# Performance work log

Hardware: AMD Instinct MI355X
Metric: run time of the kernel (lower is better)

The kernel has to match this reference:

```python
import jax, jax.numpy as jnp
import numpy as np

N_NODES = 50000
N_RAND_EDGES = 800000
NEG_SLOPE = 0.2


def gat_conv(h, src, dst, W, attn_l, attn_r, bias, res_W=None, act=False):
    # DGL GATConv semantics: fc -> per-node attn halves -> per-edge leaky_relu
    # logits -> segment softmax over destination -> weighted scatter-sum.
    N = h.shape[0]
    H, D = attn_l.shape
    feat = (h @ W).reshape(N, H, D)                      # (N,H,D)
    el = (feat * attn_l[None]).sum(-1)                   # (N,H)
    er = (feat * attn_r[None]).sum(-1)                   # (N,H)
    e = jax.nn.leaky_relu(el[src] + er[dst], NEG_SLOPE)  # (E,H)
    emax = jax.ops.segment_max(e, dst, num_segments=N)   # (N,H)
    ee = jnp.exp(e - emax[dst])                          # (E,H)
    denom = jax.ops.segment_sum(ee, dst, num_segments=N)
    alpha = ee / denom[dst]                              # (E,H)
    msg = feat[src] * alpha[:, :, None]                  # (E,H,D) dominant traffic
    rst = jax.ops.segment_sum(msg, dst, num_segments=N)  # (N,H,D)
    if res_W is not None:
        rst = rst + (h @ res_W).reshape(N, H, D)
    rst = rst + bias.reshape(1, H, D)
    if act:
        rst = jax.nn.relu(rst)
    return rst


def setup_inputs() -> dict:
    key = jax.random.key(0)
    ks = jax.random.split(key, 20)
    x = jax.random.normal(ks[0], (N_NODES, 64), dtype=jnp.float32)
    src_r = jax.random.randint(ks[1], (N_RAND_EDGES,), 0, N_NODES, dtype=jnp.int32)
    dst_r = jax.random.randint(ks[2], (N_RAND_EDGES,), 0, N_NODES, dtype=jnp.int32)
    loops = jnp.arange(N_NODES, dtype=jnp.int32)
    src = jnp.concatenate([src_r, loops])   # self-loops: no zero in-degree
    dst = jnp.concatenate([dst_r, loops])
    s = 0.1
    p = lambda k, shp: jax.random.normal(k, shp, dtype=jnp.float32) * s
    return {
        "x": x, "src": src, "dst": dst,
        # layer 1: in=64 -> hid=32, heads=4, relu, no residual
        "W1": p(ks[3], (64, 128)), "al1": p(ks[4], (4, 32)), "ar1": p(ks[5], (4, 32)),
        "b1": jnp.zeros((128,), jnp.float32),
        # layer 2: in=128 -> hid=32, heads=4, relu, residual
        "W2": p(ks[6], (128, 128)), "al2": p(ks[7], (4, 32)), "ar2": p(ks[8], (4, 32)),
        "b2": jnp.zeros((128,), jnp.float32), "resW2": p(ks[9], (128, 128)),
        # layer 3: in=128 -> out=1, heads=6, no activation, residual
        "W3": p(ks[10], (128, 6)), "al3": p(ks[11], (6, 1)), "ar3": p(ks[12], (6, 1)),
        "b3": jnp.zeros((6,), jnp.float32), "resW3": p(ks[13], (128, 6)),
    }


def reference(x, src, dst, W1, al1, ar1, b1, W2, al2, ar2, b2, resW2,
              W3, al3, ar3, b3, resW3):
    h = gat_conv(x, src, dst, W1, al1, ar1, b1, None, act=True)
    h = h.reshape(h.shape[0], -1)                        # flatten heads
    h = gat_conv(h, src, dst, W2, al2, ar2, b2, resW2, act=True)
    h = h.reshape(h.shape[0], -1)
    h = gat_conv(h, src, dst, W3, al3, ar3, b3, resW3, act=False)
    return h.mean(axis=1)                                # mean over heads -> (N, out)
```

## Files before the change

### kernel.cpp

```cpp
#include <hip/hip_runtime.h>
#include <hip/hip_fp16.h>

#define NEG 0.2f
#define BUCKET_SHIFT 7
#define CAP 3200
#define PCHUNK 4096

typedef _Float16 h8 __attribute__((ext_vector_type(8)));
typedef float f4v __attribute__((ext_vector_type(4)));

template <int K>
__global__ __launch_bounds__(256) void gemm_el_k(const float* __restrict__ A,
                                                 const float* __restrict__ W,
                                                 const float* __restrict__ al,
                                                 const float* __restrict__ ar,
                                                 __half* __restrict__ feat_h,
                                                 float* __restrict__ el,
                                                 float* __restrict__ er, int N) {
    __shared__ float As[64 * K];
    const int c = threadIdx.x & 31;
    const int rg = threadIdx.x >> 5;
    const int row0 = blockIdx.x << 6;
    const int K4 = K >> 2;

    const float4* Av = (const float4*)A;
    float4* AsV = (float4*)As;
    for (int idx = threadIdx.x; idx < 16 * K; idx += 256) {
        int rr = idx / K4, kk4 = idx - rr * K4;
        int row = row0 + rr;
        float4 v = make_float4(0.f, 0.f, 0.f, 0.f);
        if (row < N) v = Av[(size_t)row * K4 + kk4];
        AsV[rr * K4 + kk4] = v;
    }
    __syncthreads();

    const float4* Wv = (const float4*)W;
    float4 acc[8];
#pragma unroll
    for (int i = 0; i < 8; i++) acc[i] = make_float4(0.f, 0.f, 0.f, 0.f);

    for (int k4 = 0; k4 < K4; k4++) {
        float4 a[8];
#pragma unroll
        for (int i = 0; i < 8; i++) a[i] = AsV[(rg * 8 + i) * K4 + k4];
#pragma unroll
        for (int kk = 0; kk < 4; kk++) {
            float4 w = Wv[((k4 << 2) + kk) * 32 + c];
#pragma unroll
            for (int i = 0; i < 8; i++) {
                float av = kk == 0 ? a[i].x : kk == 1 ? a[i].y : kk == 2 ? a[i].z : a[i].w;
                acc[i].x += av * w.x;
                acc[i].y += av * w.y;
                acc[i].z += av * w.z;
                acc[i].w += av * w.w;
            }
        }
    }

    __half2* Fh2 = (__half2*)feat_h;
#pragma unroll
    for (int i = 0; i < 8; i++) {
        int row = row0 + rg * 8 + i;
        if (row < N) {
            size_t o = ((size_t)row << 6) + (c << 1);
            Fh2[o] = __floats2half2_rn(acc[i].x, acc[i].y);
            Fh2[o + 1] = __floats2half2_rn(acc[i].z, acc[i].w);
        }
    }

    float4 alv = ((const float4*)al)[c];
    float4 arv = ((const float4*)ar)[c];
    float pel[8], per_[8];
#pragma unroll
    for (int i = 0; i < 8; i++) {
        pel[i] = acc[i].x * alv.x + acc[i].y * alv.y + acc[i].z * alv.z + acc[i].w * alv.w;
        per_[i] = acc[i].x * arv.x + acc[i].y * arv.y + acc[i].z * arv.z + acc[i].w * arv.w;
    }
#pragma unroll
    for (int m = 1; m < 8; m <<= 1) {
#pragma unroll
        for (int i = 0; i < 8; i++) {
            pel[i] += __shfl_xor(pel[i], m);
            per_[i] += __shfl_xor(per_[i], m);
        }
    }
    if ((c & 7) == 0) {
        int h = c >> 3;
#pragma unroll
        for (int i = 0; i < 8; i++) {
            int row = row0 + rg * 8 + i;
            if (row < N) {
                el[(row << 2) + h] = pel[i];
                er[(row << 2) + h] = per_[i];
            }
        }
    }
}

__global__ __launch_bounds__(256) void wconv_k(const float* __restrict__ W2,
                                               const float* __restrict__ rW2,
                                               float4* __restrict__ W2f,
                                               float4* __restrict__ rW2f) {
    int c = blockIdx.x * 256 + threadIdx.x;
    int which = c >> 11;
    int cc = c & 2047;
    int kb = cc >> 9, rem = cc & 511, t = rem >> 6, lane = rem & 63;
    int n = (t << 4) + (lane & 15);
    int k0 = (kb << 5) + ((lane >> 4) << 3);
    const float* S = which ? rW2 : W2;
    h8 v;
#pragma unroll
    for (int i = 0; i < 8; i++) v[i] = (_Float16)S[(k0 + i) * 128 + n];
    ((h8*)(which ? rW2f : W2f))[cc] = v;
}

#define MFMA_STAGE_AND_LOOP()                                                   \
    const int tid = threadIdx.x;                                                \
    const int row0 = blockIdx.x << 6;                                           \
    for (int i = tid; i < 2048; i += 256) WsF[i] = Wf[i];                       \
    const float4* Afv = (const float4*)A;                                       \
    for (int idx = tid; idx < 1024; idx += 256) {                               \
        int r = idx >> 4, kc = idx & 15;                                        \
        float4 v = make_float4(0.f, 0.f, 0.f, 0.f);                             \
        int row = row0 + r;                                                     \
        if (row < N) v = Afv[(size_t)row * 16 + kc];                            \
        int d = ((r >> 4) * 4 + (kc >> 2)) * 64 + (kc & 3) * 16 + (r & 15);     \
        AsF[d] = v;                                                             \
    }                                                                           \
    __syncthreads();                                                            \
    const int w = tid >> 6;                                                     \
    const int lane = tid & 63;                                                  \
    const h8* Ah = (const h8*)AsF;                                              \
    const h8* Wh = (const h8*)WsF;                                              \
    f4v acc[8];                                                                 \
    _Pragma("unroll") for (int t = 0; t < 8; t++) acc[t] = (f4v){0.f, 0.f, 0.f, 0.f}; \
    _Pragma("unroll") for (int kb = 0; kb < 4; kb++) {                          \
        h8 af = Ah[(w * 4 + kb) * 64 + lane];                                   \
        _Pragma("unroll") for (int t = 0; t < 8; t++) {                         \
            h8 bf = Wh[(kb * 8 + t) * 64 + lane];                               \
            acc[t] = __builtin_amdgcn_mfma_f32_16x16x32_f16(af, bf, acc[t], 0, 0, 0); \
        }                                                                       \
    }                                                                           \
    const int c16 = lane & 15;                                                  \
    const int rg = lane >> 4;

__global__ __launch_bounds__(256) void mfma_el_k(const _Float16* __restrict__ A,
                                                 const float4* __restrict__ Wf,
                                                 const float* __restrict__ al,
                                                 const float* __restrict__ ar,
                                                 _Float16* __restrict__ feat,
                                                 float* __restrict__ el,
                                                 float* __restrict__ er, int N) {
    __shared__ float4 WsF[2048];
    __shared__ float4 AsF[1024];
    MFMA_STAGE_AND_LOOP()

    float alv[8], arv[8];
#pragma unroll
    for (int t = 0; t < 8; t++) {
        alv[t] = al[(t << 4) + c16];
        arv[t] = ar[(t << 4) + c16];
    }
    float pel[4][4], per_[4][4];
#pragma unroll
    for (int j = 0; j < 4; j++)
#pragma unroll
        for (int hh = 0; hh < 4; hh++) {
            pel[j][hh] = acc[2 * hh][j] * alv[2 * hh] + acc[2 * hh + 1][j] * alv[2 * hh + 1];
            per_[j][hh] = acc[2 * hh][j] * arv[2 * hh] + acc[2 * hh + 1][j] * arv[2 * hh + 1];
        }
#pragma unroll
    for (int m = 1; m < 16; m <<= 1)
#pragma unroll
        for (int j = 0; j < 4; j++)
#pragma unroll
            for (int hh = 0; hh < 4; hh++) {
                pel[j][hh] += __shfl_xor(pel[j][hh], m);
                per_[j][hh] += __shfl_xor(per_[j][hh], m);
            }
    if (c16 == 0) {
#pragma unroll
        for (int j = 0; j < 4; j++) {
            int row = row0 + (w << 4) + (rg << 2) + j;
            if (row < N) {
                ((float4*)el)[row] = make_float4(pel[j][0], pel[j][1], pel[j][2], pel[j][3]);
                ((float4*)er)[row] = make_float4(per_[j][0], per_[j][1], per_[j][2], per_[j][3]);
            }
        }
    }

    _Float16* As2 = (_Float16*)AsF + (w << 11);
#pragma unroll
    for (int t = 0; t < 8; t++)
#pragma unroll
        for (int j = 0; j < 4; j++)
            As2[((rg << 2) + j) * 128 + (t << 4) + c16] = (_Float16)acc[t][j];
    __asm__ volatile("s_waitcnt lgkmcnt(0)" ::: "memory");
    const float4* As2v = (const float4*)As2;
    float4* featv = (float4*)feat;
#pragma unroll
    for (int ii = 0; ii < 4; ii++) {
        int ch = ii * 64 + lane;
        int row = row0 + (w << 4) + (ch >> 4);
        if (row < N) featv[(size_t)row * 16 + (ch & 15)] = As2v[ch];
    }
}

__global__ __launch_bounds__(256) void mfma_res_k(const _Float16* __restrict__ A,
                                                  const float4* __restrict__ Wf,
                                                  const _Float16* __restrict__ rsth,
                                                  const float* __restrict__ b2,
                                                  const float* __restrict__ W3,
                                                  const float* __restrict__ resW3,
                                                  const float* __restrict__ b3,
                                                  float* __restrict__ feat3,
                                                  float* __restrict__ res3, int N) {
    __shared__ float4 WsF[2048];
    __shared__ float4 AsF[1024];
    MFMA_STAGE_AND_LOOP()

    float4* As2v = (float4*)AsF + (w << 8);
#pragma unroll
    for (int ii = 0; ii < 4; ii++) {
        int ch = ii * 64 + lane;
        int row = row0 + (w << 4) + (ch >> 4);
        float4 v = make_float4(0.f, 0.f, 0.f, 0.f);
        if (row < N) v = ((const float4*)rsth)[(size_t)row * 16 + (ch & 15)];
        As2v[ch] = v;
    }
    __asm__ volatile("s_waitcnt lgkmcnt(0)" ::: "memory");
    const _Float16* As2 = (const _Float16*)As2v;

    float b2v[8];
#pragma unroll
    for (int t = 0; t < 8; t++) b2v[t] = b2[(t << 4) + c16];

    float hv[8][4];
#pragma unroll
    for (int t = 0; t < 8; t++)
#pragma unroll
        for (int j = 0; j < 4; j++) {
            float rv = (float)As2[((rg << 2) + j) * 128 + (t << 4) + c16];
            hv[t][j] = fmaxf(acc[t][j] + rv + b2v[t], 0.f);
        }

    float f3[4][6], r3[4][6];
#pragma unroll
    for (int j = 0; j < 4; j++)
#pragma unroll
        for (int h = 0; h < 6; h++) {
            f3[j][h] = 0.f;
            r3[j][h] = 0.f;
        }
#pragma unroll
    for (int t = 0; t < 8; t++) {
        int col = (t << 4) + c16;
        const float* w3p = W3 + col * 6;
        const float* rwp = resW3 + col * 6;
#pragma unroll
        for (int h = 0; h < 6; h++) {
            float w3 = w3p[h], rw = rwp[h];
#pragma unroll
            for (int j = 0; j < 4; j++) {
                f3[j][h] = fmaf(hv[t][j], w3, f3[j][h]);
                r3[j][h] = fmaf(hv[t][j], rw, r3[j][h]);
            }
        }
    }
#pragma unroll
    for (int m = 1; m < 16; m <<= 1)
#pragma unroll
        for (int j = 0; j < 4; j++)
#pragma unroll
            for (int h = 0; h < 6; h++) {
                f3[j][h] += __shfl_xor(f3[j][h], m);
                r3[j][h] += __shfl_xor(r3[j][h], m);
            }
    if (c16 == 0) {
#pragma unroll
        for (int j = 0; j < 4; j++) {
            int row = row0 + (w << 4) + (rg << 2) + j;
            if (row < N) {
#pragma unroll
                for (int h = 0; h < 6; h++) {
                    feat3[row * 6 + h] = f3[j][h];
                    res3[row * 6 + h] = r3[j][h] + b3[h];
                }
            }
        }
    }
}

__global__ __launch_bounds__(256) void partition_k(const int* __restrict__ src,
                                                   const int* __restrict__ dst,
                                                   int* __restrict__ cursor,
                                                   unsigned* __restrict__ part,
                                                   int E, int NB) {
    __shared__ unsigned stash[PCHUNK];
    __shared__ int hist[512];
    __shared__ int base[512];
    const int tid = threadIdx.x;
    const int e0 = blockIdx.x * PCHUNK;

    for (int i = tid; i < NB; i += 256) hist[i] = 0;
    __syncthreads();

    for (int i = tid; i < PCHUNK; i += 256) {
        int e = e0 + i;
        unsigned pk = 0xFFFFFFFFu;
        if (e < E) {
            int d = dst[e];
            pk = ((unsigned)d << 16) | (unsigned)src[e];
            atomicAdd(&hist[d >> BUCKET_SHIFT], 1);
        }
        stash[i] = pk;
    }
    __syncthreads();

    for (int i = tid; i < NB; i += 256) {
        int hcnt = hist[i];
        base[i] = hcnt ? atomicAdd(&cursor[i], hcnt) : 0;
        hist[i] = 0;
    }
    __syncthreads();

    for (int i = tid; i < PCHUNK; i += 256) {
        unsigned pk = stash[i];
        if (pk != 0xFFFFFFFFu) {
            int b = pk >> (16 + BUCKET_SHIFT);
            int r = base[b] + atomicAdd(&hist[b], 1);
            if (r < CAP) part[(size_t)b * CAP + r] = pk;
        }
    }
}

__global__ __launch_bounds__(256) void bucket_csr_k(const int* __restrict__ cursor,
                                                    const unsigned* __restrict__ part,
                                                    int* __restrict__ csr_src,
                                                    int* __restrict__ row_beg,
                                                    int* __restrict__ row_end,
                                                    int N) {
    __shared__ int cnt[128], sc[128], ex[128], cur[128];
    __shared__ int lcsr[CAP];
    const int b = blockIdx.x;
    const int tid = threadIdx.x;
    int m = cursor[b];
    m = m < CAP ? m : CAP;
    if (tid < 128) cnt[tid] = 0;
    __syncthreads();

    const unsigned* pp = part + (size_t)b * CAP;
    for (int i = tid; i < m; i += 256) atomicAdd(&cnt[(pp[i] >> 16) & 127], 1);
    __syncthreads();

    if (tid < 128) sc[tid] = cnt[tid];
    __syncthreads();
    for (int off = 1; off < 128; off <<= 1) {
        int t = (tid < 128 && tid >= off) ? sc[tid - off] : 0;
        __syncthreads();
        if (tid < 128) sc[tid] += t;
        __syncthreads();
    }
    if (tid < 128) {
        ex[tid] = sc[tid] - cnt[tid];
        cur[tid] = 0;
    }
    __syncthreads();

    for (int i = tid; i < m; i += 256) {
        unsigned pk = pp[i];
        int dlo = (pk >> 16) & 127;
        int r = atomicAdd(&cur[dlo], 1);
        lcsr[ex[dlo] + r] = (int)(pk & 0xFFFFu);
    }
    __syncthreads();

    const int gbase = b * CAP;
    for (int i = tid; i < m; i += 256) csr_src[gbase + i] = lcsr[i];
    int n = (b << BUCKET_SHIFT) + tid;
    if (tid < 128 && n < N) {
        row_beg[n] = gbase + ex[tid];
        row_end[n] = gbase + sc[tid];
    }
}

template <bool BR>
__global__ __launch_bounds__(256) void pull2_k(const int* __restrict__ row_beg,
                                               const int* __restrict__ row_end,
                                               const int* __restrict__ csr_src,
                                               const float* __restrict__ el,
                                               const float* __restrict__ er,
                                               const __half* __restrict__ feat_h,
                                               const float* __restrict__ bias,
                                               __half* __restrict__ outp, int N) {
    int n = (blockIdx.x << 2) + (threadIdx.x >> 6);
    if (n >= N) return;
    unsigned l = threadIdx.x & 63;
    unsigned h = l >> 4;
    float erd = er[((unsigned)n << 2) + h];
    const __half2* feat2 = (const __half2*)feat_h;
    int beg = __builtin_amdgcn_readfirstlane(row_beg[n]);
    int end = __builtin_amdgcn_readfirstlane(row_end[n]);
    float ax = 0.f, ay = 0.f, den = 0.f;
    int p = beg;
    for (; p + 4 <= end; p += 4) {
        int s0 = csr_src[p], s1 = csr_src[p + 1];
        int s2 = csr_src[p + 2], s3 = csr_src[p + 3];
        float e0 = el[((unsigned)s0 << 2) + h];
        float e1 = el[((unsigned)s1 << 2) + h];
        float e2 = el[((unsigned)s2 << 2) + h];
        float e3 = el[((unsigned)s3 << 2) + h];
        __half2 g0 = feat2[((unsigned)s0 << 6) + l];
        __half2 g1 = feat2[((unsigned)s1 << 6) + l];
        __half2 g2 = feat2[((unsigned)s2 << 6) + l];
        __half2 g3 = feat2[((unsigned)s3 << 6) + l];
        float x0 = e0 + erd, x1 = e1 + erd, x2 = e2 + erd, x3 = e3 + erd;
        x0 = fmaxf(x0, NEG * x0);
        x1 = fmaxf(x1, NEG * x1);
        x2 = fmaxf(x2, NEG * x2);
        x3 = fmaxf(x3, NEG * x3);
        float w0 = __expf(x0), w1 = __expf(x1), w2 = __expf(x2), w3 = __expf(x3);
        float2 f0 = __half22float2(g0), f1 = __half22float2(g1);
        float2 f2 = __half22float2(g2), f3 = __half22float2(g3);
        den += (w0 + w1) + (w2 + w3);
        ax = fmaf(w0, f0.x, ax);
        ay = fmaf(w0, f0.y, ay);
        ax = fmaf(w1, f1.x, ax);
        ay = fmaf(w1, f1.y, ay);
        ax = fmaf(w2, f2.x, ax);
        ay = fmaf(w2, f2.y, ay);
        ax = fmaf(w3, f3.x, ax);
        ay = fmaf(w3, f3.y, ay);
    }
    for (; p < end; p++) {
        int s0 = csr_src[p];
        float e0 = el[((unsigned)s0 << 2) + h];
        __half2 g0 = feat2[((unsigned)s0 << 6) + l];
        float x0 = e0 + erd;
        x0 = fmaxf(x0, NEG * x0);
        float w0 = __expf(x0);
        float2 f0 = __half22float2(g0);
        den += w0;
        ax = fmaf(w0, f0.x, ax);
        ay = fmaf(w0, f0.y, ay);
    }
    float inv = 1.f / den;
    float vx = ax * inv, vy = ay * inv;
    if (BR) {
        float2 b = ((const float2*)bias)[l];
        vx = fmaxf(vx + b.x, 0.f);
        vy = fmaxf(vy + b.y, 0.f);
    }
    ((__half2*)outp)[((size_t)n << 6) + l] = __floats2half2_rn(vx, vy);
}

__global__ __launch_bounds__(256) void pull6_k(const int* __restrict__ row_beg,
                                               const int* __restrict__ row_end,
                                               const int* __restrict__ csr_src,
                                               const float* __restrict__ feat3,
                                               const float* __restrict__ al3,
                                               const float* __restrict__ ar3,
                                               const float* __restrict__ res3,
                                               float* __restrict__ rst3, int N) {
    int idx = blockIdx.x * blockDim.x + threadIdx.x;
    if (idx >= N * 6) return;
    int n = idx / 6, h = idx - n * 6;
    float a3 = al3[h], r3 = ar3[h];
    float fdr = feat3[idx] * r3;
    int beg = row_beg[n], end = row_end[n];
    float acc = 0.f, den = 0.f;
    int p = beg;
    for (; p + 2 <= end; p += 2) {
        int s0 = csr_src[p], s1 = csr_src[p + 1];
        float f0 = feat3[(unsigned)s0 * 6 + h];
        float f1 = feat3[(unsigned)s1 * 6 + h];
        float x0 = fmaf(f0, a3, fdr);
        float x1 = fmaf(f1, a3, fdr);
        x0 = fmaxf(x0, NEG * x0);
        x1 = fmaxf(x1, NEG * x1);
        float w0 = __expf(x0), w1 = __expf(x1);
        den += w0 + w1;
        acc = fmaf(w0, f0, acc);
        acc = fmaf(w1, f1, acc);
    }
    if (p < end) {
        int s0 = csr_src[p];
        float f0 = feat3[(unsigned)s0 * 6 + h];
        float x0 = fmaf(f0, a3, fdr);
        x0 = fmaxf(x0, NEG * x0);
        float w0 = __expf(x0);
        den += w0;
        acc = fmaf(w0, f0, acc);
    }
    rst3[idx] = acc / den + res3[idx];
}

__global__ __launch_bounds__(256) void final_k(const float* __restrict__ rst3,
                                               float* __restrict__ out, int N) {
    int n = blockIdx.x * blockDim.x + threadIdx.x;
    if (n >= N) return;
    const float2* r2 = (const float2*)(rst3 + n * 6);
    float2 a = r2[0], b = r2[1], c = r2[2];
    out[n] = (a.x + a.y + b.x + b.y + c.x + c.y) * (1.f / 6.f);
}

extern "C" void kernel_launch(void* const* d_in, const int* in_sizes, int n_in,
                              void* d_out, int out_size, void* d_ws, size_t ws_size,
                              hipStream_t stream) {
    const float* x = (const float*)d_in[0];
    const int* src = (const int*)d_in[1];
    const int* dst = (const int*)d_in[2];
    const float* W1 = (const float*)d_in[3];
    const float* al1 = (const float*)d_in[4];
    const float* ar1 = (const float*)d_in[5];
    const float* b1 = (const float*)d_in[6];
    const float* W2 = (const float*)d_in[7];
    const float* al2 = (const float*)d_in[8];
    const float* ar2 = (const float*)d_in[9];
    const float* b2 = (const float*)d_in[10];
    const float* resW2 = (const float*)d_in[11];
    const float* W3 = (const float*)d_in[12];
    const float* al3 = (const float*)d_in[13];
    const float* ar3 = (const float*)d_in[14];
    const float* b3 = (const float*)d_in[15];
    const float* resW3 = (const float*)d_in[16];
    float* out = (float*)d_out;

    const int N = in_sizes[0] / 64;
    const int E = in_sizes[1];
    const int NB = (N + 127) >> BUCKET_SHIFT;

    float* ws = (float*)d_ws;
    __half* featA = (__half*)ws;
    __half* h2h = (__half*)(ws + (size_t)N * 64);
    __half* rsth = (__half*)(ws + (size_t)N * 128);
    float* el = ws + (size_t)N * 192;
    float* er = el + (size_t)N * 4;
    float* feat3 = el;
    float* res3 = ws + (size_t)N * 200;
    float* rst3 = res3 + (size_t)N * 6;
    float* W2f = rst3 + (size_t)N * 6;
    float* rW2f = W2f + 8192;
    int* ip = (int*)(rW2f + 8192);
    int* cursor = ip;
    int* row_beg = cursor + 512;
    int* row_end = row_beg + N;
    unsigned* part = (unsigned*)(row_end + N);
    int* csr_src = (int*)(part + (size_t)NB * CAP);

    const int gN = (N + 255) / 256;
    const int gN64 = (N + 63) / 64;
    const int gN6 = (N * 6 + 255) / 256;
    const int gNw = (N + 3) / 4;
    const int gP = (E + PCHUNK - 1) / PCHUNK;

    hipMemsetAsync(cursor, 0, sizeof(int) * 512, stream);
    wconv_k<<<16, 256, 0, stream>>>(W2, resW2, (float4*)W2f, (float4*)rW2f);
    partition_k<<<gP, 256, 0, stream>>>(src, dst, cursor, part, E, NB);
    bucket_csr_k<<<NB, 256, 0, stream>>>(cursor, part, csr_src, row_beg, row_end, N);

    gemm_el_k<64><<<gN64, 256, 0, stream>>>(x, W1, al1, ar1, featA, el, er, N);
    pull2_k<true><<<gNw, 256, 0, stream>>>(row_beg, row_end, csr_src, el, er,
                                           featA, b1, h2h, N);

    mfma_el_k<<<gN64, 256, 0, stream>>>((const _Float16*)h2h, (const float4*)W2f,
                                        al2, ar2, (_Float16*)featA, el, er, N);
    pull2_k<false><<<gNw, 256, 0, stream>>>(row_beg, row_end, csr_src, el, er,
                                            featA, nullptr, rsth, N);
    mfma_res_k<<<gN64, 256, 0, stream>>>((const _Float16*)h2h, (const float4*)rW2f,
                                         (const _Float16*)rsth, b2, W3, resW3, b3,
                                         feat3, res3, N);

    pull6_k<<<gN6, 256, 0, stream>>>(row_beg, row_end, csr_src, feat3, al3, ar3,
                                     res3, rst3, N);
    final_k<<<gN, 256, 0, stream>>>(rst3, out, N);
}
```

Before: 259.9 us.

## Merge independent setup kernels and fuse layer-3 pull with head mean

```diff
diff --git a/kernel.cpp b/kernel.cpp
--- a/kernel.cpp
+++ b/kernel.cpp
@@ -9,18 +9,133 @@
 typedef _Float16 h8 __attribute__((ext_vector_type(8)));
 typedef float f4v __attribute__((ext_vector_type(4)));
 
-template <int K>
-__global__ __launch_bounds__(256) void gemm_el_k(const float* __restrict__ A,
-                                                 const float* __restrict__ W,
-                                                 const float* __restrict__ al,
-                                                 const float* __restrict__ ar,
-                                                 __half* __restrict__ feat_h,
-                                                 float* __restrict__ el,
-                                                 float* __restrict__ er, int N) {
-    __shared__ float As[64 * K];
+
+__device__ __forceinline__ void wconv_dev(int bid, const float* __restrict__ W2,
+                                          const float* __restrict__ rW2,
+                                          float4* __restrict__ W2f,
+                                          float4* __restrict__ rW2f) {
+    int c = bid * 256 + threadIdx.x;
+    int which = c >> 11;
+    int cc = c & 2047;
+    int kb = cc >> 9, rem = cc & 511, t = rem >> 6, lane = rem & 63;
+    int n = (t << 4) + (lane & 15);
+    int k0 = (kb << 5) + ((lane >> 4) << 3);
+    const float* S = which ? rW2 : W2;
+    h8 v;
+#pragma unroll
+    for (int i = 0; i < 8; i++) v[i] = (_Float16)S[(k0 + i) * 128 + n];
+    ((h8*)(which ? rW2f : W2f))[cc] = v;
+}
+
+__device__ __forceinline__ void partition_dev(char* smem, int bid,
+                                              const int* __restrict__ src,
+                                              const int* __restrict__ dst,
+                                              int* __restrict__ cursor,
+                                              unsigned* __restrict__ part,
+                                              int E, int NB) {
+    unsigned* stash = (unsigned*)smem;
+    int* hist = (int*)(smem + PCHUNK * 4);
+    int* base = hist + 512;
+    const int tid = threadIdx.x;
+    const int e0 = bid * PCHUNK;
+
+    for (int i = tid; i < NB; i += 256) hist[i] = 0;
+    __syncthreads();
+
+    for (int i = tid; i < PCHUNK; i += 256) {
+        int e = e0 + i;
+        unsigned pk = 0xFFFFFFFFu;
+        if (e < E) {
+            int d = dst[e];
+            pk = ((unsigned)d << 16) | (unsigned)src[e];
+            atomicAdd(&hist[d >> BUCKET_SHIFT], 1);
+        }
+        stash[i] = pk;
+    }
+    __syncthreads();
+
+    for (int i = tid; i < NB; i += 256) {
+        int hcnt = hist[i];
+        base[i] = hcnt ? atomicAdd(&cursor[i], hcnt) : 0;
+        hist[i] = 0;
+    }
+    __syncthreads();
+
+    for (int i = tid; i < PCHUNK; i += 256) {
+        unsigned pk = stash[i];
+        if (pk != 0xFFFFFFFFu) {
+            int b = pk >> (16 + BUCKET_SHIFT);
+            int r = base[b] + atomicAdd(&hist[b], 1);
+            if (r < CAP) part[(size_t)b * CAP + r] = pk;
+        }
+    }
+}
+
+__device__ __forceinline__ void bucket_dev(char* smem, int b,
+                                           const int* __restrict__ cursor,
+                                           const unsigned* __restrict__ part,
+                                           int* __restrict__ csr_src,
+                                           int* __restrict__ row_beg,
+                                           int* __restrict__ row_end, int N) {
+    int* cnt = (int*)smem;
+    int* sc = cnt + 128;
+    int* ex = sc + 128;
+    int* cur = ex + 128;
+    int* lcsr = cur + 128;
+    const int tid = threadIdx.x;
+    int m = cursor[b];
+    m = m < CAP ? m : CAP;
+    if (tid < 128) cnt[tid] = 0;
+    __syncthreads();
+
+    const unsigned* pp = part + (size_t)b * CAP;
+    for (int i = tid; i < m; i += 256) atomicAdd(&cnt[(pp[i] >> 16) & 127], 1);
+    __syncthreads();
+
+    if (tid < 128) sc[tid] = cnt[tid];
+    __syncthreads();
+    for (int off = 1; off < 128; off <<= 1) {
+        int t = (tid < 128 && tid >= off) ? sc[tid - off] : 0;
+        __syncthreads();
+        if (tid < 128) sc[tid] += t;
+        __syncthreads();
+    }
+    if (tid < 128) {
+        ex[tid] = sc[tid] - cnt[tid];
+        cur[tid] = 0;
+    }
+    __syncthreads();
+
+    for (int i = tid; i < m; i += 256) {
+        unsigned pk = pp[i];
+        int dlo = (pk >> 16) & 127;
+        int r = atomicAdd(&cur[dlo], 1);
+        lcsr[ex[dlo] + r] = (int)(pk & 0xFFFFu);
+    }
+    __syncthreads();
+
+    const int gbase = b * CAP;
+    for (int i = tid; i < m; i += 256) csr_src[gbase + i] = lcsr[i];
+    int n = (b << BUCKET_SHIFT) + tid;
+    if (tid < 128 && n < N) {
+        row_beg[n] = gbase + ex[tid];
+        row_end[n] = gbase + sc[tid];
+    }
+}
+
+__device__ __forceinline__ void gemm_el_dev(char* smem, int bid,
+                                            const float* __restrict__ A,
+                                            const float* __restrict__ W,
+                                            const float* __restrict__ al,
+                                            const float* __restrict__ ar,
+                                            __half* __restrict__ feat_h,
+                                            float* __restrict__ el,
+                                            float* __restrict__ er, int N) {
+    constexpr int K = 64;
+    float* As = (float*)smem;
     const int c = threadIdx.x & 31;
     const int rg = threadIdx.x >> 5;
-    const int row0 = blockIdx.x << 6;
+    const int row0 = bid << 6;
     const int K4 = K >> 2;
 
     const float4* Av = (const float4*)A;
@@ -97,21 +212,39 @@
     }
 }
 
-__global__ __launch_bounds__(256) void wconv_k(const float* __restrict__ W2,
-                                               const float* __restrict__ rW2,
-                                               float4* __restrict__ W2f,
-                                               float4* __restrict__ rW2f) {
-    int c = blockIdx.x * 256 + threadIdx.x;
-    int which = c >> 11;
-    int cc = c & 2047;
-    int kb = cc >> 9, rem = cc & 511, t = rem >> 6, lane = rem & 63;
-    int n = (t << 4) + (lane & 15);
-    int k0 = (kb << 5) + ((lane >> 4) << 3);
-    const float* S = which ? rW2 : W2;
-    h8 v;
-#pragma unroll
-    for (int i = 0; i < 8; i++) v[i] = (_Float16)S[(k0 + i) * 128 + n];
-    ((h8*)(which ? rW2f : W2f))[cc] = v;
+__global__ __launch_bounds__(256) void stage1_k(const float* __restrict__ W2,
+                                                const float* __restrict__ rW2,
+                                                float4* __restrict__ W2f,
+                                                float4* __restrict__ rW2f,
+                                                const int* __restrict__ src,
+                                                const int* __restrict__ dst,
+                                                int* __restrict__ cursor,
+                                                unsigned* __restrict__ part,
+                                                int E, int NB) {
+    __shared__ __align__(16) char smem[20480];
+    if (blockIdx.x < 16)
+        wconv_dev(blockIdx.x, W2, rW2, W2f, rW2f);
+    else
+        partition_dev(smem, blockIdx.x - 16, src, dst, cursor, part, E, NB);
+}
+
+__global__ __launch_bounds__(256) void stage2_k(const int* __restrict__ cursor,
+                                                const unsigned* __restrict__ part,
+                                                int* __restrict__ csr_src,
+                                                int* __restrict__ row_beg,
+                                                int* __restrict__ row_end, int NB,
+                                                const float* __restrict__ x,
+                                                const float* __restrict__ W1,
+                                                const float* __restrict__ al1,
+                                                const float* __restrict__ ar1,
+                                                __half* __restrict__ featA,
+                                                float* __restrict__ el,
+                                                float* __restrict__ er, int N) {
+    __shared__ __align__(16) char smem[16384];
+    if ((int)blockIdx.x < NB)
+        bucket_dev(smem, blockIdx.x, cursor, part, csr_src, row_beg, row_end, N);
+    else
+        gemm_el_dev(smem, blockIdx.x - NB, x, W1, al1, ar1, featA, el, er, N);
 }
 
 #define MFMA_STAGE_AND_LOOP()                                                   \
@@ -288,99 +421,6 @@
                 }
             }
         }
-    }
-}
-
-__global__ __launch_bounds__(256) void partition_k(const int* __restrict__ src,
-                                                   const int* __restrict__ dst,
-                                                   int* __restrict__ cursor,
-                                                   unsigned* __restrict__ part,
-                                                   int E, int NB) {
-    __shared__ unsigned stash[PCHUNK];
-    __shared__ int hist[512];
-    __shared__ int base[512];
-    const int tid = threadIdx.x;
-    const int e0 = blockIdx.x * PCHUNK;
-
-    for (int i = tid; i < NB; i += 256) hist[i] = 0;
-    __syncthreads();
-
-    for (int i = tid; i < PCHUNK; i += 256) {
-        int e = e0 + i;
-        unsigned pk = 0xFFFFFFFFu;
-        if (e < E) {
-            int d = dst[e];
-            pk = ((unsigned)d << 16) | (unsigned)src[e];
-            atomicAdd(&hist[d >> BUCKET_SHIFT], 1);
-        }
-        stash[i] = pk;
-    }
-    __syncthreads();
-
-    for (int i = tid; i < NB; i += 256) {
-        int hcnt = hist[i];
-        base[i] = hcnt ? atomicAdd(&cursor[i], hcnt) : 0;
-        hist[i] = 0;
-    }
-    __syncthreads();
-
-    for (int i = tid; i < PCHUNK; i += 256) {
-        unsigned pk = stash[i];
-        if (pk != 0xFFFFFFFFu) {
-            int b = pk >> (16 + BUCKET_SHIFT);
-            int r = base[b] + atomicAdd(&hist[b], 1);
-            if (r < CAP) part[(size_t)b * CAP + r] = pk;
-        }
-    }
-}
-
-__global__ __launch_bounds__(256) void bucket_csr_k(const int* __restrict__ cursor,
-                                                    const unsigned* __restrict__ part,
-                                                    int* __restrict__ csr_src,
-                                                    int* __restrict__ row_beg,
-                                                    int* __restrict__ row_end,
-                                                    int N) {
-    __shared__ int cnt[128], sc[128], ex[128], cur[128];
-    __shared__ int lcsr[CAP];
-    const int b = blockIdx.x;
-    const int tid = threadIdx.x;
-    int m = cursor[b];
-    m = m < CAP ? m : CAP;
-    if (tid < 128) cnt[tid] = 0;
-    __syncthreads();
-
-    const unsigned* pp = part + (size_t)b * CAP;
-    for (int i = tid; i < m; i += 256) atomicAdd(&cnt[(pp[i] >> 16) & 127], 1);
-    __syncthreads();
-
-    if (tid < 128) sc[tid] = cnt[tid];
-    __syncthreads();
-    for (int off = 1; off < 128; off <<= 1) {
-        int t = (tid < 128 && tid >= off) ? sc[tid - off] : 0;
-        __syncthreads();
-        if (tid < 128) sc[tid] += t;
-        __syncthreads();
-    }
-    if (tid < 128) {
-        ex[tid] = sc[tid] - cnt[tid];
-        cur[tid] = 0;
-    }
-    __syncthreads();
-
-    for (int i = tid; i < m; i += 256) {
-        unsigned pk = pp[i];
-        int dlo = (pk >> 16) & 127;
-        int r = atomicAdd(&cur[dlo], 1);
-        lcsr[ex[dlo] + r] = (int)(pk & 0xFFFFu);
-    }
-    __syncthreads();
-
-    const int gbase = b * CAP;
-    for (int i = tid; i < m; i += 256) csr_src[gbase + i] = lcsr[i];
-    int n = (b << BUCKET_SHIFT) + tid;
-    if (tid < 128 && n < N) {
-        row_beg[n] = gbase + ex[tid];
-        row_end[n] = gbase + sc[tid];
     }
 }
 
@@ -454,54 +494,41 @@
     ((__half2*)outp)[((size_t)n << 6) + l] = __floats2half2_rn(vx, vy);
 }
 
-__global__ __launch_bounds__(256) void pull6_k(const int* __restrict__ row_beg,
-                                               const int* __restrict__ row_end,
-                                               const int* __restrict__ csr_src,
-                                               const float* __restrict__ feat3,
-                                               const float* __restrict__ al3,
-                                               const float* __restrict__ ar3,
-                                               const float* __restrict__ res3,
-                                               float* __restrict__ rst3, int N) {
-    int idx = blockIdx.x * blockDim.x + threadIdx.x;
-    if (idx >= N * 6) return;
-    int n = idx / 6, h = idx - n * 6;
-    float a3 = al3[h], r3 = ar3[h];
-    float fdr = feat3[idx] * r3;
-    int beg = row_beg[n], end = row_end[n];
-    float acc = 0.f, den = 0.f;
-    int p = beg;
-    for (; p + 2 <= end; p += 2) {
-        int s0 = csr_src[p], s1 = csr_src[p + 1];
-        float f0 = feat3[(unsigned)s0 * 6 + h];
-        float f1 = feat3[(unsigned)s1 * 6 + h];
-        float x0 = fmaf(f0, a3, fdr);
-        float x1 = fmaf(f1, a3, fdr);
-        x0 = fmaxf(x0, NEG * x0);
-        x1 = fmaxf(x1, NEG * x1);
-        float w0 = __expf(x0), w1 = __expf(x1);
-        den += w0 + w1;
-        acc = fmaf(w0, f0, acc);
-        acc = fmaf(w1, f1, acc);
-    }
-    if (p < end) {
-        int s0 = csr_src[p];
-        float f0 = feat3[(unsigned)s0 * 6 + h];
-        float x0 = fmaf(f0, a3, fdr);
-        x0 = fmaxf(x0, NEG * x0);
-        float w0 = __expf(x0);
-        den += w0;
-        acc = fmaf(w0, f0, acc);
-    }
-    rst3[idx] = acc / den + res3[idx];
-}
-
-__global__ __launch_bounds__(256) void final_k(const float* __restrict__ rst3,
-                                               float* __restrict__ out, int N) {
+__global__ __launch_bounds__(256) void pull6f_k(const int* __restrict__ row_beg,
+                                                const int* __restrict__ row_end,
+                                                const int* __restrict__ csr_src,
+                                                const float* __restrict__ feat3,
+                                                const float* __restrict__ al3,
+                                                const float* __restrict__ ar3,
+                                                const float* __restrict__ res3,
+                                                float* __restrict__ out, int N) {
     int n = blockIdx.x * blockDim.x + threadIdx.x;
     if (n >= N) return;
-    const float2* r2 = (const float2*)(rst3 + n * 6);
-    float2 a = r2[0], b = r2[1], c = r2[2];
-    out[n] = (a.x + a.y + b.x + b.y + c.x + c.y) * (1.f / 6.f);
+    float a3[6], fdr[6], acc[6], den[6];
+#pragma unroll
+    for (int h = 0; h < 6; h++) {
+        a3[h] = al3[h];
+        fdr[h] = feat3[n * 6 + h] * ar3[h];
+        acc[h] = 0.f;
+        den[h] = 0.f;
+    }
+    int beg = row_beg[n], end = row_end[n];
+    for (int p = beg; p < end; p++) {
+        int s = csr_src[p];
+#pragma unroll
+        for (int h = 0; h < 6; h++) {
+            float f = feat3[(unsigned)s * 6 + h];
+            float x = fmaf(f, a3[h], fdr[h]);
+            x = fmaxf(x, NEG * x);
+            float w = __expf(x);
+            den[h] += w;
+            acc[h] = fmaf(w, f, acc[h]);
+        }
+    }
+    float m = 0.f;
+#pragma unroll
+    for (int h = 0; h < 6; h++) m += acc[h] / den[h] + res3[n * 6 + h];
+    out[n] = m * (1.f / 6.f);
 }
 
 extern "C" void kernel_launch(void* const* d_in, const int* in_sizes, int n_in,
@@ -538,8 +565,7 @@
     float* er = el + (size_t)N * 4;
     float* feat3 = el;
     float* res3 = ws + (size_t)N * 200;
-    float* rst3 = res3 + (size_t)N * 6;
-    float* W2f = rst3 + (size_t)N * 6;
+    float* W2f = res3 + (size_t)N * 6;
     float* rW2f = W2f + 8192;
     int* ip = (int*)(rW2f + 8192);
     int* cursor = ip;
@@ -550,16 +576,15 @@
 
     const int gN = (N + 255) / 256;
     const int gN64 = (N + 63) / 64;
-    const int gN6 = (N * 6 + 255) / 256;
     const int gNw = (N + 3) / 4;
     const int gP = (E + PCHUNK - 1) / PCHUNK;
 
     hipMemsetAsync(cursor, 0, sizeof(int) * 512, stream);
-    wconv_k<<<16, 256, 0, stream>>>(W2, resW2, (float4*)W2f, (float4*)rW2f);
-    partition_k<<<gP, 256, 0, stream>>>(src, dst, cursor, part, E, NB);
-    bucket_csr_k<<<NB, 256, 0, stream>>>(cursor, part, csr_src, row_beg, row_end, N);
-
-    gemm_el_k<64><<<gN64, 256, 0, stream>>>(x, W1, al1, ar1, featA, el, er, N);
+    stage1_k<<<16 + gP, 256, 0, stream>>>(W2, resW2, (float4*)W2f, (float4*)rW2f,
+                                          src, dst, cursor, part, E, NB);
+    stage2_k<<<NB + gN64, 256, 0, stream>>>(cursor, part, csr_src, row_beg, row_end,
+                                            NB, x, W1, al1, ar1, featA, el, er, N);
+
     pull2_k<true><<<gNw, 256, 0, stream>>>(row_beg, row_end, csr_src, el, er,
                                            featA, b1, h2h, N);
 
@@ -571,7 +596,6 @@
                                          (const _Float16*)rsth, b2, W3, resW3, b3,
                                          feat3, res3, N);
 
-    pull6_k<<<gN6, 256, 0, stream>>>(row_beg, row_end, csr_src, feat3, al3, ar3,
-                                     res3, rst3, N);
-    final_k<<<gN, 256, 0, stream>>>(rst3, out, N);
-}
+    pull6f_k<<<gN, 256, 0, stream>>>(row_beg, row_end, csr_src, feat3, al3, ar3,
+                                     res3, out, N);
+}
```

New measurement: 253.7 us. -2.4%, faster.
